# Kernel optimization log

Hardware: AMD Instinct MI355X
Metric: run time of the kernel (lower is better)

The kernel has to match this reference:

```python
import jax, jax.numpy as jnp
import numpy as np

H = 256        # hidden_size
NC = 15        # num_components (decode steps)
V = 26         # vocab_size
E = 64         # embed_dim
B = 65536      # batch


def setup_inputs() -> dict:
    key = jax.random.key(0)
    ks = jax.random.split(key, 8)
    return {
        "context": jax.random.normal(ks[0], (B, H), jnp.float32),
        "embed_table": (jax.random.normal(ks[1], (V, E), jnp.float32) * 0.02),
        "start_embed": (jax.random.normal(ks[2], (E,), jnp.float32) * 0.02),
        "Wp": jax.random.normal(ks[3], (H, H), jnp.float32) / np.sqrt(H),
        "bp": jnp.zeros((H,), jnp.float32),
        "Wi": jax.random.normal(ks[4], (H + E, 4 * H), jnp.float32) / np.sqrt(H + E),
        "Wh": jax.random.normal(ks[5], (H, 4 * H), jnp.float32) / np.sqrt(H),
        "bh": jnp.zeros((4 * H,), jnp.float32),
        "Wo": jax.random.normal(ks[6], (H, V), jnp.float32) / np.sqrt(H),
        "bo": jnp.zeros((V,), jnp.float32),
        "seed": 0,
    }


def _lstm_step(c, h, x, Wi, Wh, bh):
    # flax OptimizedLSTMCell: fused gates, order i, f, g, o; bias on hidden path only
    gates = x @ Wi + h @ Wh + bh            # (B, 4H)
    i, f, g, o = jnp.split(gates, 4, axis=-1)
    c_new = jax.nn.sigmoid(f) * c + jax.nn.sigmoid(i) * jnp.tanh(g)
    h_new = jax.nn.sigmoid(o) * jnp.tanh(c_new)
    return c_new, h_new


def reference(context, embed_table, start_embed, Wp, bp, Wi, Wh, bh, Wo, bo, seed):
    b = context.shape[0]
    h = jnp.tanh(context @ Wp + bp)          # init_proj + tanh
    c = jnp.zeros_like(h)
    prev = jnp.broadcast_to(start_embed, (b, start_embed.shape[0]))
    keys = jax.random.split(jax.random.key(seed), NC)  # one subkey per decode step

    def step(carry, k):
        c, h, prev = carry
        x = jnp.concatenate([context, prev], axis=-1)   # (B, H+E)
        c, h = _lstm_step(c, h, x, Wi, Wh, bh)
        logits = h @ Wo + bo                            # (B, V)
        tok = jax.random.categorical(k, logits, axis=-1)  # (B,) int
        prev = embed_table[tok]                         # embedding lookup
        return (c, h, prev), (logits, tok)

    _, (logits, samples) = jax.lax.scan(step, (c, h, prev), keys)
    # scan stacks on axis 0 (time); move to (B, NC, ...)
    return jnp.transpose(logits, (1, 0, 2)), jnp.transpose(samples, (1, 0))
```

## Files before the change

### kernel.cpp

```cpp
#include <hip/hip_runtime.h>
#include <cstdint>
#include <cstddef>

#define NROWS 16
#define NTHR  256
#define HSZ   256
#define ESZ   64
#define VSZ   26
#define NCOMP 15
#define BATCH 65536

__device__ __forceinline__ uint32_t rotl32(uint32_t v, int d) {
  return (v << d) | (v >> (32 - d));
}

__device__ __forceinline__ void tf2x32(uint32_t kA, uint32_t kB,
                                       uint32_t& x0, uint32_t& x1) {
  uint32_t kC = kA ^ kB ^ 0x1BD11BDAu;
  x0 += kA; x1 += kB;
#define TFR(r) { x0 += x1; x1 = rotl32(x1, r); x1 ^= x0; }
  TFR(13) TFR(15) TFR(26) TFR(6)
  x0 += kB; x1 += kC + 1u;
  TFR(17) TFR(29) TFR(16) TFR(24)
  x0 += kC; x1 += kA + 2u;
  TFR(13) TFR(15) TFR(26) TFR(6)
  x0 += kA; x1 += kB + 3u;
  TFR(17) TFR(29) TFR(16) TFR(24)
  x0 += kB; x1 += kC + 4u;
  TFR(13) TFR(15) TFR(26) TFR(6)
  x0 += kC; x1 += kA + 5u;
#undef TFR
}

__device__ __forceinline__ float xla_tanh(float x) {
  #pragma clang fp contract(off)
  float ax = fabsf(x);
  float xc = fminf(fmaxf(x, -7.90531110763549805f), 7.90531110763549805f);
  float x2 = xc * xc;
  float nu = -2.76076847742355e-16f;
  nu = x2 * nu + 2.00018790482477e-13f;
  nu = x2 * nu + -8.60467152213735e-11f;
  nu = x2 * nu + 5.12229709037114e-08f;
  nu = x2 * nu + 1.48572235717979e-05f;
  nu = x2 * nu + 6.37261928875436e-04f;
  nu = x2 * nu + 4.89352455891786e-03f;
  nu = xc * nu;
  float de = 1.19825839466702e-06f;
  de = x2 * de + 1.18534705686654e-04f;
  de = x2 * de + 2.26843463243900e-03f;
  de = x2 * de + 4.89352518554385e-03f;
  float r = nu / de;
  return (ax < 0.0004f) ? x : r;
}

__device__ __forceinline__ float xla_sigmoid(float x) {
  #pragma clang fp contract(off)
  return 0.5f + 0.5f * xla_tanh(0.5f * x);
}

__device__ __forceinline__ float xla_log(float x) {
  #pragma clang fp contract(off)
  uint32_t bits = __float_as_uint(x);
  int ei = (int)(bits >> 23) - 126;
  float m = __uint_as_float((bits & 0x007FFFFFu) | 0x3F000000u);
  bool lt = m < 0.707106781186547524f;
  float ee = (float)ei - (lt ? 1.0f : 0.0f);
  float mm = (m - 1.0f) + (lt ? m : 0.0f);
  float x2 = mm * mm;
  float x3 = x2 * mm;
  float y  = __builtin_fmaf(7.0376836292E-2f,  mm, -1.1514610310E-1f);
  float y1 = __builtin_fmaf(-1.2420140846E-1f, mm,  1.4249322787E-1f);
  float y2 = __builtin_fmaf(2.0000714765E-1f,  mm, -2.4999993993E-1f);
  y  = __builtin_fmaf(y,  mm, 1.1676998740E-1f);
  y1 = __builtin_fmaf(y1, mm, -1.6668057665E-1f);
  y2 = __builtin_fmaf(y2, mm, 3.3333331174E-1f);
  y  = __builtin_fmaf(y, x3, y1);
  y  = __builtin_fmaf(y, x3, y2);
  y  = y * x3;
  float t1 = ee * -2.12194440e-4f;
  float t2 = 0.5f * x2;
  y  = y + t1;
  mm = mm - t2;
  float t3 = ee * 0.693359375f;
  mm = mm + y;
  mm = mm + t3;
  return mm;
}

__device__ __forceinline__ void chain4(float* aI, float* aF, float* aG, float* aO,
                                       const float* lds, const float* W, int u, int nk) {
  const float* w = W + u;
  for (int k = 0; k < nk; ++k) {
    float wI = w[0], wF = w[256], wG = w[512], wO = w[768];
    w += 1024;
    #pragma unroll
    for (int rq = 0; rq < 4; ++rq) {
      float hv[4];
      *(float4*)hv = *(const float4*)(lds + k * 16 + rq * 4);
      #pragma unroll
      for (int j = 0; j < 4; ++j) {
        int r = rq * 4 + j;
        aI[r] = __builtin_fmaf(hv[j], wI, aI[r]);
        aF[r] = __builtin_fmaf(hv[j], wF, aF[r]);
        aG[r] = __builtin_fmaf(hv[j], wG, aG[r]);
        aO[r] = __builtin_fmaf(hv[j], wO, aO[r]);
      }
    }
  }
}

__device__ __forceinline__ void chain4v(float* aI, float* aF, float* aG, float* aO,
                                        const float* lds, const float4* W4, int u, int nk) {
  const float4* w = W4 + u;
  #pragma unroll 2
  for (int k = 0; k < nk; ++k) {
    float4 wv = w[(size_t)k * 256];
    #pragma unroll
    for (int rq = 0; rq < 4; ++rq) {
      float hv[4];
      *(float4*)hv = *(const float4*)(lds + k * 16 + rq * 4);
      #pragma unroll
      for (int j = 0; j < 4; ++j) {
        int r = rq * 4 + j;
        aI[r] = __builtin_fmaf(hv[j], wv.x, aI[r]);
        aF[r] = __builtin_fmaf(hv[j], wv.y, aF[r]);
        aG[r] = __builtin_fmaf(hv[j], wv.z, aG[r]);
        aO[r] = __builtin_fmaf(hv[j], wv.w, aO[r]);
      }
    }
  }
}

__global__ void repack_w(const float* __restrict__ W, float4* __restrict__ W4, int n) {
  int i = blockIdx.x * blockDim.x + threadIdx.x;
  if (i < n) {
    int k = i >> 8, u = i & 255;
    const float* src = W + (size_t)k * 1024 + u;
    W4[i] = make_float4(src[0], src[256], src[512], src[768]);
  }
}

__global__ __launch_bounds__(NTHR, 2) void belief_main(
    const float* __restrict__ ctx, const float* __restrict__ embed,
    const float* __restrict__ start_e, const float* __restrict__ Wp,
    const float* __restrict__ bp, const float* __restrict__ Wi,
    const float* __restrict__ Wh, const float* __restrict__ bh,
    const float* __restrict__ Wo, const float* __restrict__ bo,
    const int* __restrict__ seedp, float* __restrict__ out,
    const float4* __restrict__ Wi4, const float4* __restrict__ Wh4, int packed) {
  __shared__ __align__(16) float hT[HSZ * NROWS];
  __shared__ __align__(16) float ctxT[HSZ * NROWS];
  __shared__ __align__(16) float prevT[ESZ * NROWS];
  __shared__ __align__(16) float woLds[HSZ * VSZ];
  __shared__ float boLds[VSZ];
  __shared__ float scores[NROWS * VSZ];
  __shared__ int tokLds[NROWS];
  __shared__ uint32_t skLds[NCOMP * 2];

  const int t = threadIdx.x;
  const int b0 = blockIdx.x * NROWS;

  #pragma unroll
  for (int r = 0; r < NROWS; ++r)
    ctxT[t * NROWS + r] = ctx[(size_t)(b0 + r) * HSZ + t];
  for (int i = t; i < HSZ * VSZ; i += NTHR) woLds[i] = Wo[i];
  if (t < VSZ) boLds[t] = bo[t];
  for (int i = t; i < ESZ * NROWS; i += NTHR) prevT[i] = start_e[i >> 4];
  if (t < NCOMP) {
    uint32_t x0 = 0u, x1 = (uint32_t)t;
    tf2x32(0u, (uint32_t)seedp[0], x0, x1);
    skLds[2 * t] = x0; skLds[2 * t + 1] = x1;
  }
  __syncthreads();

  float c[NROWS];
  {
    float acc[NROWS];
    #pragma unroll
    for (int r = 0; r < NROWS; ++r) acc[r] = 0.0f;
    const float* wp = Wp + t;
    for (int m = 0; m < HSZ; ++m) {
      float w = wp[(size_t)m * HSZ];
      #pragma unroll
      for (int rq = 0; rq < 4; ++rq) {
        float hv[4];
        *(float4*)hv = *(const float4*)&ctxT[m * NROWS + rq * 4];
        #pragma unroll
        for (int j = 0; j < 4; ++j)
          acc[rq * 4 + j] = __builtin_fmaf(hv[j], w, acc[rq * 4 + j]);
      }
    }
    float bpv = bp[t];
    #pragma unroll
    for (int r = 0; r < NROWS; ++r) {
      float s = acc[r] + bpv;
      hT[t * NROWS + r] = xla_tanh(s);
      c[r] = 0.0f;
    }
  }

  float pI[16], pF[16], pG[16], pO[16];
  #pragma unroll
  for (int r = 0; r < 16; ++r) { pI[r] = 0.f; pF[r] = 0.f; pG[r] = 0.f; pO[r] = 0.f; }
  if (packed) chain4v(pI, pF, pG, pO, ctxT, Wi4, t, HSZ);
  else        chain4 (pI, pF, pG, pO, ctxT, Wi,  t, HSZ);
  __syncthreads();

  const float bhI = bh[t], bhF = bh[256 + t], bhG = bh[512 + t], bhO = bh[768 + t];
  const float*  WiP  = Wi  + (size_t)HSZ * 1024;
  const float4* WiP4 = Wi4 + (size_t)HSZ * 256;

  for (int s = 0; s < NCOMP; ++s) {
    float aI[16], aF[16], aG[16], aO[16];
    #pragma unroll
    for (int r = 0; r < 16; ++r) { aI[r] = pI[r]; aF[r] = pF[r]; aG[r] = pG[r]; aO[r] = pO[r]; }
    if (packed) chain4v(aI, aF, aG, aO, prevT, WiP4, t, ESZ);
    else        chain4 (aI, aF, aG, aO, prevT, WiP,  t, ESZ);

    float bI[16], bF[16], bG[16], bO[16];
    #pragma unroll
    for (int r = 0; r < 16; ++r) { bI[r] = 0.f; bF[r] = 0.f; bG[r] = 0.f; bO[r] = 0.f; }
    if (packed) chain4v(bI, bF, bG, bO, hT, Wh4, t, HSZ);
    else        chain4 (bI, bF, bG, bO, hT, Wh,  t, HSZ);

    float hnew[16];
    {
      #pragma clang fp contract(off)
      #pragma unroll
      for (int r = 0; r < 16; ++r) {
        float gi = (aI[r] + bI[r]) + bhI;
        float gf = (aF[r] + bF[r]) + bhF;
        float gg = (aG[r] + bG[r]) + bhG;
        float go = (aO[r] + bO[r]) + bhO;
        float si = xla_sigmoid(gi);
        float sf = xla_sigmoid(gf);
        float tg = xla_tanh(gg);
        float so = xla_sigmoid(go);
        float cn = sf * c[r] + si * tg;
        c[r] = cn;
        hnew[r] = so * xla_tanh(cn);
      }
    }
    __syncthreads();
    #pragma unroll
    for (int r = 0; r < 16; ++r) hT[t * NROWS + r] = hnew[r];
    __syncthreads();

    uint32_t sk0 = skLds[2 * s], sk1 = skLds[2 * s + 1];
    for (int p = t; p < NROWS * VSZ; p += NTHR) {
      int r = p / VSZ, v = p - r * VSZ;
      float acc = 0.0f;
      for (int k = 0; k < HSZ; ++k)
        acc = __builtin_fmaf(hT[k * NROWS + r], woLds[k * VSZ + v], acc);
      float logit = acc + boLds[v];
      out[(size_t)(b0 + r) * (NCOMP * VSZ) + s * VSZ + v] = logit;

      uint32_t n = (uint32_t)(b0 + r) * VSZ + (uint32_t)v;
      uint32_t x0 = 0u, x1 = n;
      tf2x32(sk0, sk1, x0, x1);
      uint32_t rb = x0 ^ x1;
      float f = __uint_as_float((rb >> 9) | 0x3F800000u) - 1.0f;
      float uu;
      {
        #pragma clang fp contract(off)
        uu = f + 1.17549435082228751e-38f;
      }
      uu = fmaxf(1.17549435082228751e-38f, uu);
      float l1 = xla_log(uu);
      float g = -xla_log(-l1);
      {
        #pragma clang fp contract(off)
        scores[r * VSZ + v] = g + logit;
      }
    }
    __syncthreads();

    if (t < NROWS) {
      float mbest = scores[t * VSZ];
      int ibest = 0;
      for (int v = 1; v < VSZ; ++v) {
        float sc = scores[t * VSZ + v];
        if (sc > mbest) { mbest = sc; ibest = v; }
      }
      tokLds[t] = ibest;
      out[(size_t)BATCH * (NCOMP * VSZ) + (size_t)(b0 + t) * NCOMP + s] = (float)ibest;
    }
    __syncthreads();
    if (s < NCOMP - 1) {
      for (int i = t; i < ESZ * NROWS; i += NTHR) {
        int e = i >> 4, r = i & 15;
        prevT[i] = embed[tokLds[r] * ESZ + e];
      }
    }
    __syncthreads();
  }
}

extern "C" void kernel_launch(void* const* d_in, const int* in_sizes, int n_in,
                              void* d_out, int out_size, void* d_ws, size_t ws_size,
                              hipStream_t stream) {
  const float* ctx     = (const float*)d_in[0];
  const float* embed   = (const float*)d_in[1];
  const float* start_e = (const float*)d_in[2];
  const float* Wp      = (const float*)d_in[3];
  const float* bp      = (const float*)d_in[4];
  const float* Wi      = (const float*)d_in[5];
  const float* Wh      = (const float*)d_in[6];
  const float* bh      = (const float*)d_in[7];
  const float* Wo      = (const float*)d_in[8];
  const float* bo      = (const float*)d_in[9];
  const int*   seedp   = (const int*)d_in[10];
  float* out = (float*)d_out;

  size_t wi4_elems = (size_t)(HSZ + ESZ) * 256;
  size_t wh4_elems = (size_t)HSZ * 256;
  size_t need = (wi4_elems + wh4_elems) * sizeof(float4);
  int packed = (d_ws != nullptr && ws_size >= need) ? 1 : 0;
  float4* Wi4 = (float4*)d_ws;
  float4* Wh4 = Wi4 + wi4_elems;

  if (packed) {
    int nWi = (int)wi4_elems, nWh = (int)wh4_elems;
    hipLaunchKernelGGL(repack_w, dim3((nWi + 255) / 256), dim3(256), 0, stream, Wi, Wi4, nWi);
    hipLaunchKernelGGL(repack_w, dim3((nWh + 255) / 256), dim3(256), 0, stream, Wh, Wh4, nWh);
  }

  hipLaunchKernelGGL(belief_main, dim3(BATCH / NROWS), dim3(NTHR), 0, stream,
                     ctx, embed, start_e, Wp, bp, Wi, Wh, bh, Wo, bo, seedp,
                     out, Wi4, Wh4, packed);
}
```

Measured before the change: 10.52 ms.

## Halve rows per block, overlay shared buffers, read Wo from global for occupancy

Each block now handles 8 batch rows instead of 16, and launch bounds go from 2 to 4 blocks per CU. This cuts accumulator registers and lets more waves hide weight-load latency. Shared memory shrinks: the ctx, prev-embedding, scores, token and subkey buffers share one overlay buffer, and the Wo copy in LDS is dropped so logits read Wo from global/cache. The packed flag becomes a template parameter. The trade-off is that each weight load is reused across half as many rows, roughly doubling weight traffic per row, and Wo is now read from global memory on every step.

```diff
diff --git a/kernel.cpp b/kernel.cpp
--- a/kernel.cpp
+++ b/kernel.cpp
@@ -2,7 +2,7 @@
 #include <cstdint>
 #include <cstddef>
 
-#define NROWS 16
+#define NROWS 8
 #define NTHR  256
 #define HSZ   256
 #define ESZ   64
@@ -87,45 +87,39 @@
   return mm;
 }
 
-__device__ __forceinline__ void chain4(float* aI, float* aF, float* aG, float* aO,
-                                       const float* lds, const float* W, int u, int nk) {
-  const float* w = W + u;
-  for (int k = 0; k < nk; ++k) {
-    float wI = w[0], wF = w[256], wG = w[512], wO = w[768];
-    w += 1024;
-    #pragma unroll
-    for (int rq = 0; rq < 4; ++rq) {
-      float hv[4];
-      *(float4*)hv = *(const float4*)(lds + k * 16 + rq * 4);
+template<bool PACKED>
+__device__ __forceinline__ void chain8(float* aI, float* aF, float* aG, float* aO,
+                                       const float* lds, const float4* W4,
+                                       const float* W, int u, int nk) {
+  if constexpr (PACKED) {
+    const float4* w = W4 + u;
+    for (int k = 0; k < nk; ++k) {
+      float4 wv = w[(size_t)k * 256];
+      float hv[8];
+      *(float4*)&hv[0] = *(const float4*)(lds + k * 8);
+      *(float4*)&hv[4] = *(const float4*)(lds + k * 8 + 4);
       #pragma unroll
-      for (int j = 0; j < 4; ++j) {
-        int r = rq * 4 + j;
-        aI[r] = __builtin_fmaf(hv[j], wI, aI[r]);
-        aF[r] = __builtin_fmaf(hv[j], wF, aF[r]);
-        aG[r] = __builtin_fmaf(hv[j], wG, aG[r]);
-        aO[r] = __builtin_fmaf(hv[j], wO, aO[r]);
-      }
-    }
-  }
-}
-
-__device__ __forceinline__ void chain4v(float* aI, float* aF, float* aG, float* aO,
-                                        const float* lds, const float4* W4, int u, int nk) {
-  const float4* w = W4 + u;
-  #pragma unroll 2
-  for (int k = 0; k < nk; ++k) {
-    float4 wv = w[(size_t)k * 256];
-    #pragma unroll
-    for (int rq = 0; rq < 4; ++rq) {
-      float hv[4];
-      *(float4*)hv = *(const float4*)(lds + k * 16 + rq * 4);
+      for (int j = 0; j < 8; ++j) {
+        aI[j] = __builtin_fmaf(hv[j], wv.x, aI[j]);
+        aF[j] = __builtin_fmaf(hv[j], wv.y, aF[j]);
+        aG[j] = __builtin_fmaf(hv[j], wv.z, aG[j]);
+        aO[j] = __builtin_fmaf(hv[j], wv.w, aO[j]);
+      }
+    }
+  } else {
+    const float* w = W + u;
+    for (int k = 0; k < nk; ++k) {
+      float wI = w[0], wF = w[256], wG = w[512], wO = w[768];
+      w += 1024;
+      float hv[8];
+      *(float4*)&hv[0] = *(const float4*)(lds + k * 8);
+      *(float4*)&hv[4] = *(const float4*)(lds + k * 8 + 4);
       #pragma unroll
-      for (int j = 0; j < 4; ++j) {
-        int r = rq * 4 + j;
-        aI[r] = __builtin_fmaf(hv[j], wv.x, aI[r]);
-        aF[r] = __builtin_fmaf(hv[j], wv.y, aF[r]);
-        aG[r] = __builtin_fmaf(hv[j], wv.z, aG[r]);
-        aO[r] = __builtin_fmaf(hv[j], wv.w, aO[r]);
+      for (int j = 0; j < 8; ++j) {
+        aI[j] = __builtin_fmaf(hv[j], wI, aI[j]);
+        aF[j] = __builtin_fmaf(hv[j], wF, aF[j]);
+        aG[j] = __builtin_fmaf(hv[j], wG, aG[j]);
+        aO[j] = __builtin_fmaf(hv[j], wO, aO[j]);
       }
     }
   }
@@ -140,22 +134,24 @@
   }
 }
 
-__global__ __launch_bounds__(NTHR, 2) void belief_main(
+template<bool PACKED>
+__global__ __launch_bounds__(NTHR, 4) void belief_main(
     const float* __restrict__ ctx, const float* __restrict__ embed,
     const float* __restrict__ start_e, const float* __restrict__ Wp,
     const float* __restrict__ bp, const float* __restrict__ Wi,
     const float* __restrict__ Wh, const float* __restrict__ bh,
     const float* __restrict__ Wo, const float* __restrict__ bo,
     const int* __restrict__ seedp, float* __restrict__ out,
-    const float4* __restrict__ Wi4, const float4* __restrict__ Wh4, int packed) {
+    const float4* __restrict__ Wi4, const float4* __restrict__ Wh4) {
   __shared__ __align__(16) float hT[HSZ * NROWS];
-  __shared__ __align__(16) float ctxT[HSZ * NROWS];
-  __shared__ __align__(16) float prevT[ESZ * NROWS];
-  __shared__ __align__(16) float woLds[HSZ * VSZ];
+  __shared__ __align__(16) float ovl[HSZ * NROWS];
   __shared__ float boLds[VSZ];
-  __shared__ float scores[NROWS * VSZ];
-  __shared__ int tokLds[NROWS];
-  __shared__ uint32_t skLds[NCOMP * 2];
+
+  float* ctxT   = ovl;
+  float* prevT  = ovl;
+  float* scores = ovl + ESZ * NROWS;
+  int*   tokLds = (int*)(ovl + ESZ * NROWS + NROWS * VSZ);
+  uint32_t* skLds = (uint32_t*)(tokLds + NROWS);
 
   const int t = threadIdx.x;
   const int b0 = blockIdx.x * NROWS;
@@ -163,9 +159,39 @@
   #pragma unroll
   for (int r = 0; r < NROWS; ++r)
     ctxT[t * NROWS + r] = ctx[(size_t)(b0 + r) * HSZ + t];
-  for (int i = t; i < HSZ * VSZ; i += NTHR) woLds[i] = Wo[i];
   if (t < VSZ) boLds[t] = bo[t];
-  for (int i = t; i < ESZ * NROWS; i += NTHR) prevT[i] = start_e[i >> 4];
+  __syncthreads();
+
+  float c[NROWS];
+  {
+    float acc[NROWS];
+    #pragma unroll
+    for (int r = 0; r < NROWS; ++r) acc[r] = 0.0f;
+    const float* wp = Wp + t;
+    for (int m = 0; m < HSZ; ++m) {
+      float w = wp[(size_t)m * HSZ];
+      float hv[8];
+      *(float4*)&hv[0] = *(const float4*)&ctxT[m * NROWS];
+      *(float4*)&hv[4] = *(const float4*)&ctxT[m * NROWS + 4];
+      #pragma unroll
+      for (int j = 0; j < 8; ++j) acc[j] = __builtin_fmaf(hv[j], w, acc[j]);
+    }
+    float bpv = bp[t];
+    #pragma unroll
+    for (int r = 0; r < NROWS; ++r) {
+      float s = acc[r] + bpv;
+      hT[t * NROWS + r] = xla_tanh(s);
+      c[r] = 0.0f;
+    }
+  }
+
+  float pI[NROWS], pF[NROWS], pG[NROWS], pO[NROWS];
+  #pragma unroll
+  for (int r = 0; r < NROWS; ++r) { pI[r] = 0.f; pF[r] = 0.f; pG[r] = 0.f; pO[r] = 0.f; }
+  chain8<PACKED>(pI, pF, pG, pO, ctxT, Wi4, Wi, t, HSZ);
+  __syncthreads();
+
+  for (int i = t; i < ESZ * NROWS; i += NTHR) prevT[i] = start_e[i >> 3];
   if (t < NCOMP) {
     uint32_t x0 = 0u, x1 = (uint32_t)t;
     tf2x32(0u, (uint32_t)seedp[0], x0, x1);
@@ -173,61 +199,26 @@
   }
   __syncthreads();
 
-  float c[NROWS];
-  {
-    float acc[NROWS];
-    #pragma unroll
-    for (int r = 0; r < NROWS; ++r) acc[r] = 0.0f;
-    const float* wp = Wp + t;
-    for (int m = 0; m < HSZ; ++m) {
-      float w = wp[(size_t)m * HSZ];
-      #pragma unroll
-      for (int rq = 0; rq < 4; ++rq) {
-        float hv[4];
-        *(float4*)hv = *(const float4*)&ctxT[m * NROWS + rq * 4];
-        #pragma unroll
-        for (int j = 0; j < 4; ++j)
-          acc[rq * 4 + j] = __builtin_fmaf(hv[j], w, acc[rq * 4 + j]);
-      }
-    }
-    float bpv = bp[t];
-    #pragma unroll
-    for (int r = 0; r < NROWS; ++r) {
-      float s = acc[r] + bpv;
-      hT[t * NROWS + r] = xla_tanh(s);
-      c[r] = 0.0f;
-    }
-  }
-
-  float pI[16], pF[16], pG[16], pO[16];
-  #pragma unroll
-  for (int r = 0; r < 16; ++r) { pI[r] = 0.f; pF[r] = 0.f; pG[r] = 0.f; pO[r] = 0.f; }
-  if (packed) chain4v(pI, pF, pG, pO, ctxT, Wi4, t, HSZ);
-  else        chain4 (pI, pF, pG, pO, ctxT, Wi,  t, HSZ);
-  __syncthreads();
-
   const float bhI = bh[t], bhF = bh[256 + t], bhG = bh[512 + t], bhO = bh[768 + t];
   const float*  WiP  = Wi  + (size_t)HSZ * 1024;
   const float4* WiP4 = Wi4 + (size_t)HSZ * 256;
 
   for (int s = 0; s < NCOMP; ++s) {
-    float aI[16], aF[16], aG[16], aO[16];
-    #pragma unroll
-    for (int r = 0; r < 16; ++r) { aI[r] = pI[r]; aF[r] = pF[r]; aG[r] = pG[r]; aO[r] = pO[r]; }
-    if (packed) chain4v(aI, aF, aG, aO, prevT, WiP4, t, ESZ);
-    else        chain4 (aI, aF, aG, aO, prevT, WiP,  t, ESZ);
-
-    float bI[16], bF[16], bG[16], bO[16];
-    #pragma unroll
-    for (int r = 0; r < 16; ++r) { bI[r] = 0.f; bF[r] = 0.f; bG[r] = 0.f; bO[r] = 0.f; }
-    if (packed) chain4v(bI, bF, bG, bO, hT, Wh4, t, HSZ);
-    else        chain4 (bI, bF, bG, bO, hT, Wh,  t, HSZ);
-
-    float hnew[16];
+    float bI[NROWS], bF[NROWS], bG[NROWS], bO[NROWS];
+    #pragma unroll
+    for (int r = 0; r < NROWS; ++r) { bI[r] = 0.f; bF[r] = 0.f; bG[r] = 0.f; bO[r] = 0.f; }
+    chain8<PACKED>(bI, bF, bG, bO, hT, Wh4, Wh, t, HSZ);
+
+    float aI[NROWS], aF[NROWS], aG[NROWS], aO[NROWS];
+    #pragma unroll
+    for (int r = 0; r < NROWS; ++r) { aI[r] = pI[r]; aF[r] = pF[r]; aG[r] = pG[r]; aO[r] = pO[r]; }
+    chain8<PACKED>(aI, aF, aG, aO, prevT, WiP4, WiP, t, ESZ);
+
+    float hnew[NROWS];
     {
       #pragma clang fp contract(off)
       #pragma unroll
-      for (int r = 0; r < 16; ++r) {
+      for (int r = 0; r < NROWS; ++r) {
         float gi = (aI[r] + bI[r]) + bhI;
         float gf = (aF[r] + bF[r]) + bhF;
         float gg = (aG[r] + bG[r]) + bhG;
@@ -243,15 +234,15 @@
     }
     __syncthreads();
     #pragma unroll
-    for (int r = 0; r < 16; ++r) hT[t * NROWS + r] = hnew[r];
+    for (int r = 0; r < NROWS; ++r) hT[t * NROWS + r] = hnew[r];
     __syncthreads();
 
     uint32_t sk0 = skLds[2 * s], sk1 = skLds[2 * s + 1];
-    for (int p = t; p < NROWS * VSZ; p += NTHR) {
-      int r = p / VSZ, v = p - r * VSZ;
+    if (t < NROWS * VSZ) {
+      int r = t / VSZ, v = t - r * VSZ;
       float acc = 0.0f;
       for (int k = 0; k < HSZ; ++k)
-        acc = __builtin_fmaf(hT[k * NROWS + r], woLds[k * VSZ + v], acc);
+        acc = __builtin_fmaf(hT[k * NROWS + r], Wo[k * VSZ + v], acc);
       float logit = acc + boLds[v];
       out[(size_t)(b0 + r) * (NCOMP * VSZ) + s * VSZ + v] = logit;
 
@@ -288,7 +279,7 @@
     __syncthreads();
     if (s < NCOMP - 1) {
       for (int i = t; i < ESZ * NROWS; i += NTHR) {
-        int e = i >> 4, r = i & 15;
+        int e = i >> 3, r = i & 7;
         prevT[i] = embed[tokLds[r] * ESZ + e];
       }
     }
@@ -323,9 +314,12 @@
     int nWi = (int)wi4_elems, nWh = (int)wh4_elems;
     hipLaunchKernelGGL(repack_w, dim3((nWi + 255) / 256), dim3(256), 0, stream, Wi, Wi4, nWi);
     hipLaunchKernelGGL(repack_w, dim3((nWh + 255) / 256), dim3(256), 0, stream, Wh, Wh4, nWh);
-  }
-
-  hipLaunchKernelGGL(belief_main, dim3(BATCH / NROWS), dim3(NTHR), 0, stream,
-                     ctx, embed, start_e, Wp, bp, Wi, Wh, bh, Wo, bo, seedp,
-                     out, Wi4, Wh4, packed);
-}
+    hipLaunchKernelGGL(belief_main<true>, dim3(BATCH / NROWS), dim3(NTHR), 0, stream,
+                       ctx, embed, start_e, Wp, bp, Wi, Wh, bh, Wo, bo, seedp,
+                       out, Wi4, Wh4);
+  } else {
+    hipLaunchKernelGGL(belief_main<false>, dim3(BATCH / NROWS), dim3(NTHR), 0, stream,
+                       ctx, embed, start_e, Wp, bp, Wi, Wh, bh, Wo, bo, seedp,
+                       out, Wi4, Wh4);
+  }
+}
```

Measured after the change: 12.08 ms. 14.9% more time.
